# Kernel optimization log

Hardware: AMD Instinct MI355X
Metric: run time of the kernel (lower is better)

Reference implementation:

```python
import jax, jax.numpy as jnp
import numpy as np

N_EMBD = 768
N_HEAD = 12
HEAD_DIM = N_EMBD // N_HEAD


def setup_inputs() -> dict:
    key = jax.random.key(0)
    k1, k2, k3 = jax.random.split(key, 3)
    B, T, C = 4, 2048, N_EMBD
    x = jax.random.normal(k1, (B, T, C), dtype=jnp.float32)
    # c_attn: torch Linear(C, 3C) -> store as (C, 3C) for x @ W
    w_attn = jax.random.normal(k2, (C, 3 * C), dtype=jnp.float32) * (1.0 / np.sqrt(C))
    b_attn = jax.random.normal(k3, (3 * C,), dtype=jnp.float32) * 0.02
    return {"x": x, "w_attn": w_attn, "b_attn": b_attn}


def reference(x, w_attn, b_attn):
    B, T, C = x.shape
    H, D = N_HEAD, HEAD_DIM
    scale = 1.0 / np.sqrt(D).astype(np.float32)

    qkv = x @ w_attn + b_attn                      # (B, T, 3C)
    q, k, v = jnp.split(qkv, 3, axis=-1)
    q = q.reshape(B, T, H, D).transpose(0, 2, 1, 3)  # (B, H, T, D)
    k = k.reshape(B, T, H, D).transpose(0, 2, 1, 3)
    v = v.reshape(B, T, H, D).transpose(0, 2, 1, 3)

    att = jnp.einsum('bhid,bhjd->bhij', q, k) * scale  # (B, H, T, T)
    causal = jnp.tril(jnp.ones((T, T), dtype=bool))
    # masked positions -> -inf -> relu -> 0; kept positions -> relu(scaled score)
    att = jnp.where(causal, jnp.maximum(att, 0.0), 0.0)

    y = jnp.einsum('bhij,bhjd->bhid', att, v)      # (B, H, T, D)
    y = y.transpose(0, 2, 1, 3).reshape(B, T, C)
    return y
```

## Files before the change

### kernel.cpp

```cpp
#include <hip/hip_runtime.h>
#include <hip/hip_bf16.h>

typedef short bf16x8 __attribute__((ext_vector_type(8)));
typedef float f32x4  __attribute__((ext_vector_type(4)));
typedef unsigned short u16x4 __attribute__((ext_vector_type(4)));

#define CDIM   768
#define NQKV   2304
#define MROWS  8192
#define TSEQ   2048
#define HD     64
#define NHEAD  12
#define BHTOT  48

__device__ __forceinline__ unsigned short f2bf(float f) {
    unsigned int x;
    __builtin_memcpy(&x, &f, 4);
    unsigned int r = (x + 0x7fffu + ((x >> 16) & 1u)) >> 16;
    return (unsigned short)r;
}

__device__ __forceinline__ unsigned int pkbf(float a, float b) {
    unsigned int ua, ub;
    __builtin_memcpy(&ua, &a, 4);
    __builtin_memcpy(&ub, &b, 4);
    return __builtin_amdgcn_perm(ua + 0x8000u, ub + 0x8000u, 0x03020706u);
}

__device__ __forceinline__ f32x4 mfma16(bf16x8 a, bf16x8 b, f32x4 c) {
    return __builtin_amdgcn_mfma_f32_16x16x32_bf16(a, b, c, 0, 0, 0);
}

__device__ __forceinline__ void gl_lds16(const unsigned short* g, unsigned short* l) {
    __builtin_amdgcn_global_load_lds(
        (__attribute__((address_space(1))) void*)(g),
        (__attribute__((address_space(3))) void*)(l),
        16, 0, 0);
}

__global__ __launch_bounds__(256) void prep(
    const float* __restrict__ X, const float* __restrict__ W,
    unsigned short* __restrict__ Xb, unsigned short* __restrict__ Wt)
{
    const int tid = threadIdx.x, blk = blockIdx.x;
    if (blk < 432) {
        __shared__ __align__(16) unsigned short tile[64][72];
        const int bx = blk % 36, by = blk / 36;
#pragma unroll
        for (int c = 0; c < 4; c++) {
            int chunk = tid + 256 * c;
            int r = chunk >> 4, cc = chunk & 15;
            f32x4 v = *(const f32x4*)(W + (size_t)(by * 64 + r) * NQKV + bx * 64 + cc * 4);
#pragma unroll
            for (int j = 0; j < 4; j++) tile[cc * 4 + j][r] = f2bf(v[j]);
        }
        __syncthreads();
#pragma unroll
        for (int c = 0; c < 2; c++) {
            int chunk = tid + 256 * c;
            int r = chunk >> 3, cc = chunk & 7;
            bf16x8 v;
#pragma unroll
            for (int j = 0; j < 8; j++) v[j] = (short)tile[r][cc * 8 + j];
            *(bf16x8*)(Wt + (size_t)(bx * 64 + r) * CDIM + by * 64 + cc * 8) = v;
        }
    }
    for (size_t i4 = (size_t)blk * 256 + tid; i4 < (size_t)(MROWS * CDIM / 4);
         i4 += (size_t)448 * 256) {
        f32x4 v = *(const f32x4*)(X + i4 * 4);
        u16x4 o;
#pragma unroll
        for (int j = 0; j < 4; j++) o[j] = f2bf(v[j]);
        *(u16x4*)(Xb + i4 * 4) = o;
    }
}

#define BK 64

__global__ __launch_bounds__(512, 4) void qkv_gemm(
    const unsigned short* __restrict__ X,
    const unsigned short* __restrict__ Wt,
    const float* __restrict__ Bias,
    unsigned short* __restrict__ Q,
    unsigned short* __restrict__ Km,
    unsigned short* __restrict__ Vt)
{
    __shared__ __align__(16) unsigned short As[256 * BK];
    __shared__ __align__(16) unsigned short Bs[128 * BK];
    const int tid  = threadIdx.x;
    const int wave = tid >> 6, lane = tid & 63;
    const int quad = lane >> 4, m16 = lane & 15;
    const int wr = wave >> 1, wc = wave & 1;

    const int t   = blockIdx.x;
    const int xcd = t & 7, s = t >> 3;
    const int m0  = (xcd * 4 + (s & 3)) * 256;
    const int n0  = (s >> 2) * 128;

    f32x4 acc[4][4];
#pragma unroll
    for (int i = 0; i < 4; i++)
#pragma unroll
        for (int j = 0; j < 4; j++) acc[i][j] = f32x4{0.f, 0.f, 0.f, 0.f};

    const unsigned short* xb = X + (size_t)m0 * CDIM;
    const unsigned short* wb = Wt + (size_t)n0 * CDIM;

    const int spos = lane & 7;
    const int rb = m16 & 7;
    int arow[4], brow[2];
#pragma unroll
    for (int c = 0; c < 4; c++) arow[c] = (wave * 256 + c * 64 + lane) >> 3;
#pragma unroll
    for (int c = 0; c < 2; c++) brow[c] = (wave * 128 + c * 64 + lane) >> 3;

    for (int k0 = 0; k0 < CDIM; k0 += BK) {
#pragma unroll
        for (int c = 0; c < 4; c++) {
            int row = arow[c], ch = spos ^ (row & 7);
            gl_lds16(xb + (size_t)row * CDIM + k0 + ch * 8, As + wave * 2048 + c * 512);
        }
#pragma unroll
        for (int c = 0; c < 2; c++) {
            int row = brow[c], ch = spos ^ (row & 7);
            gl_lds16(wb + (size_t)row * CDIM + k0 + ch * 8, Bs + wave * 1024 + c * 512);
        }
        __syncthreads();
#pragma unroll
        for (int ks = 0; ks < 2; ks++) {
            bf16x8 af[4], bfg[4];
#pragma unroll
            for (int u = 0; u < 4; u++) {
                int rowa = wr * 64 + u * 16 + m16;
                int rowb = wc * 64 + u * 16 + m16;
                int pos = (ks * 4 + quad) ^ rb;
                af[u]  = *(const bf16x8*)(As + rowa * 64 + pos * 8);
                bfg[u] = *(const bf16x8*)(Bs + rowb * 64 + pos * 8);
            }
#pragma unroll
            for (int i = 0; i < 4; i++)
#pragma unroll
                for (int j = 0; j < 4; j++)
                    acc[i][j] = mfma16(af[i], bfg[j], acc[i][j]);
        }
        __syncthreads();
    }

    const int region = n0 / CDIM;
    const float qscale = (region == 0) ? 0.125f : 1.0f;
#pragma unroll
    for (int i = 0; i < 4; i++) {
        int row = m0 + wr * 64 + i * 16 + quad * 4;
#pragma unroll
        for (int j = 0; j < 4; j++) {
            int gcol = n0 + wc * 64 + j * 16 + m16;
            int cc = gcol - region * CDIM;
            int h = cc >> 6, d = cc & 63;
            float bv = Bias[gcol];
#pragma unroll
            for (int r = 0; r < 4; r++) {
                int gm = row + r;
                int b = gm >> 11, tq = gm & 2047;
                int bh = b * NHEAD + h;
                unsigned short o = f2bf((acc[i][j][r] + bv) * qscale);
                if (region == 0)      Q[((size_t)bh * TSEQ + tq) * HD + d] = o;
                else if (region == 1) Km[((size_t)bh * TSEQ + tq) * HD + d] = o;
                else                  Vt[((size_t)bh * HD + d) * TSEQ + tq] = o;
            }
        }
    }
}

#define LDSK 0
#define LDSV 8192

__global__ __launch_bounds__(256, 4) void attn(
    const unsigned short* __restrict__ Q,
    const unsigned short* __restrict__ Kmat,
    const unsigned short* __restrict__ Vt,
    float* __restrict__ Out)
{
    __shared__ __align__(16) unsigned short S[16384];

    const int tid  = threadIdx.x;
    const int wave = tid >> 6, lane = tid & 63;
    const int q4 = lane >> 4, m16 = lane & 15;
    const int q8 = m16 >> 2, m3 = m16 & 3;

    const int xcd = blockIdx.x & 7;
    const int idx = blockIdx.x >> 3;
    const int bh  = xcd * 6 + (idx % 6);
    const int it  = 15 - (idx / 6);
    const int i0  = it * 128;

    const unsigned short* qb = Q    + (size_t)bh * TSEQ * HD;
    const unsigned short* kb = Kmat + (size_t)bh * TSEQ * HD;
    const unsigned short* vb = Vt   + (size_t)bh * HD * TSEQ;

    bf16x8 qf[2][2];
#pragma unroll
    for (int si = 0; si < 2; si++)
#pragma unroll
        for (int ks = 0; ks < 2; ks++)
            qf[si][ks] = *(const bf16x8*)(qb +
                (size_t)(i0 + wave * 32 + si * 16 + m16) * HD + ks * 32 + q4 * 8);

    f32x4 oacc[2][4];
#pragma unroll
    for (int si = 0; si < 2; si++)
#pragma unroll
        for (int dn = 0; dn < 4; dn++) oacc[si][dn] = f32x4{0.f, 0.f, 0.f, 0.f};

    const int fr  = ((q8 & 1) << 2) | m3;
    const int kx0 = (q4 ^ fr) * 8;
    const int kx1 = kx0 ^ 32;
    const int krb = (q8 * 8 + m3) * 64;

    for (int jt = 0; jt <= it; jt++) {
        const int j0 = jt * 128;
#pragma unroll
        for (int cc = 0; cc < 4; cc++) {
            int cs = wave * 4 + cc;
            {
                int rowK = cs * 8 + (lane >> 3);
                int chK  = (lane & 7) ^ ((((rowK >> 3) & 1) << 2) | (rowK & 3));
                gl_lds16(kb + (size_t)(j0 + rowK) * HD + chK * 8, &S[LDSK] + cs * 512);
            }
            {
                int dV  = cs * 4 + (lane >> 4);
                int chV = (m16 & 8) | ((m16 ^ dV) & 7);
                gl_lds16(vb + (size_t)dV * TSEQ + j0 + chV * 8, &S[LDSV] + cs * 512);
            }
        }
        __syncthreads();

        const bool diag = (jt == it);
#pragma unroll
        for (int kk = 0; kk < 4; kk++) {
            const int kb0 = kk * 2048 + krb;
            bf16x8 kf_e0 = *(const bf16x8*)(&S[LDSK] + kb0 + kx0);
            bf16x8 kf_e1 = *(const bf16x8*)(&S[LDSK] + kb0 + kx1);
            bf16x8 kf_o0 = *(const bf16x8*)(&S[LDSK] + kb0 + 256 + kx0);
            bf16x8 kf_o1 = *(const bf16x8*)(&S[LDSK] + kb0 + 256 + kx1);

            f32x4 sacc[2][2];
#pragma unroll
            for (int o = 0; o < 2; o++)
#pragma unroll
                for (int si = 0; si < 2; si++) sacc[o][si] = f32x4{0.f, 0.f, 0.f, 0.f};
#pragma unroll
            for (int si = 0; si < 2; si++) {
                sacc[0][si] = mfma16(kf_e0, qf[si][0], sacc[0][si]);
                sacc[0][si] = mfma16(kf_e1, qf[si][1], sacc[0][si]);
                sacc[1][si] = mfma16(kf_o0, qf[si][0], sacc[1][si]);
                sacc[1][si] = mfma16(kf_o1, qf[si][1], sacc[1][si]);
            }

            unsigned int pk[2][2][2];
#pragma unroll
            for (int o = 0; o < 2; o++)
#pragma unroll
                for (int si = 0; si < 2; si++) {
                    f32x4 v = sacc[o][si];
                    if (diag) {
#pragma unroll
                        for (int r = 0; r < 4; r++) {
                            int gj = kk * 32 + q4 * 8 + o * 4 + r;
                            int gi = wave * 32 + si * 16 + m16;
                            if (gj > gi) v[r] = 0.f;
                        }
                    }
#pragma unroll
                    for (int r = 0; r < 4; r++) v[r] = fmaxf(v[r], 0.f);
                    pk[o][si][0] = pkbf(v[0], v[1]);
                    pk[o][si][1] = pkbf(v[2], v[3]);
                }

#pragma unroll
            for (int dn = 0; dn < 4; dn++) {
                int vsw = ((kk * 4 + q4) ^ (m16 & 7)) * 8;
                bf16x8 vf = *(const bf16x8*)(&S[LDSV] + (dn * 16 + m16) * 128 + vsw);
#pragma unroll
                for (int si = 0; si < 2; si++) {
                    union { bf16x8 v; unsigned int u[4]; } af;
                    af.u[0] = pk[0][si][0];
                    af.u[1] = pk[0][si][1];
                    af.u[2] = pk[1][si][0];
                    af.u[3] = pk[1][si][1];
                    oacc[si][dn] = mfma16(af.v, vf, oacc[si][dn]);
                }
            }
        }
        __syncthreads();
    }

    const int b = bh / NHEAD, h = bh % NHEAD;
#pragma unroll
    for (int si = 0; si < 2; si++) {
        int ri = i0 + wave * 32 + si * 16 + q4 * 4;
#pragma unroll
        for (int dn = 0; dn < 4; dn++) {
            int d = dn * 16 + m16;
#pragma unroll
            for (int r = 0; r < 4; r++) {
                Out[((size_t)b * TSEQ + ri + r) * CDIM + h * HD + d] = oacc[si][dn][r];
            }
        }
    }
}

extern "C" void kernel_launch(void* const* d_in, const int* in_sizes, int n_in,
                              void* d_out, int out_size, void* d_ws, size_t ws_size,
                              hipStream_t stream) {
    const float* X    = (const float*)d_in[0];
    const float* W    = (const float*)d_in[1];
    const float* Bias = (const float*)d_in[2];
    float* out = (float*)d_out;

    unsigned short* Xb = (unsigned short*)d_ws;
    unsigned short* Wt = Xb + (size_t)MROWS * CDIM;
    unsigned short* Q  = Wt + (size_t)NQKV * CDIM;
    unsigned short* Km = Q  + (size_t)BHTOT * TSEQ * HD;
    unsigned short* Vt = Km + (size_t)BHTOT * TSEQ * HD;

    hipLaunchKernelGGL(prep, dim3(448), dim3(256), 0, stream, X, W, Xb, Wt);
    hipLaunchKernelGGL(qkv_gemm, dim3(576), dim3(512), 0, stream,
                       Xb, Wt, Bias, Q, Km, Vt);
    hipLaunchKernelGGL(attn, dim3(BHTOT * 16), dim3(256), 0, stream, Q, Km, Vt, out);
}
```

Measured before the change: 178.0 us.

## Double attention query tile to 256 rows with 8 waves sharing K/V tiles

Each attention block now covers 256 query rows with 512 threads (8 waves) instead of 128 rows with 4 waves. Each K/V tile staged in LDS is therefore reused by twice as many query rows, and each wave loads half as many chunks. The causal mask check becomes per-wave, since the diagonal now spans two key tiles. The cost is fewer, larger blocks (384), which gives coarser causal load balancing and wasted MFMA work on fully masked tiles for the lower waves.

Result: no change. 181.3 us (+1.8%).

```diff
diff --git a/kernel.cpp b/kernel.cpp
--- a/kernel.cpp
+++ b/kernel.cpp
@@ -174,7 +174,7 @@
 #define LDSK 0
 #define LDSV 8192
 
-__global__ __launch_bounds__(256, 4) void attn(
+__global__ __launch_bounds__(512, 4) void attn(
     const unsigned short* __restrict__ Q,
     const unsigned short* __restrict__ Kmat,
     const unsigned short* __restrict__ Vt,
@@ -188,10 +188,11 @@
     const int q8 = m16 >> 2, m3 = m16 & 3;
 
     const int xcd = blockIdx.x & 7;
-    const int idx = blockIdx.x >> 3;
-    const int bh  = xcd * 6 + (idx % 6);
-    const int it  = 15 - (idx / 6);
-    const int i0  = it * 128;
+    const int u   = blockIdx.x >> 3;
+    const int bh  = xcd * 6 + (u % 6);
+    const int it2 = 7 - (u / 6);
+    const int i0  = it2 * 256;
+    const int iw  = i0 + wave * 32;
 
     const unsigned short* qb = Q    + (size_t)bh * TSEQ * HD;
     const unsigned short* kb = Kmat + (size_t)bh * TSEQ * HD;
@@ -203,7 +204,7 @@
 #pragma unroll
         for (int ks = 0; ks < 2; ks++)
             qf[si][ks] = *(const bf16x8*)(qb +
-                (size_t)(i0 + wave * 32 + si * 16 + m16) * HD + ks * 32 + q4 * 8);
+                (size_t)(iw + si * 16 + m16) * HD + ks * 32 + q4 * 8);
 
     f32x4 oacc[2][4];
 #pragma unroll
@@ -216,11 +217,12 @@
     const int kx1 = kx0 ^ 32;
     const int krb = (q8 * 8 + m3) * 64;
 
-    for (int jt = 0; jt <= it; jt++) {
+    const int njt = 2 * it2 + 2;
+    for (int jt = 0; jt < njt; jt++) {
         const int j0 = jt * 128;
 #pragma unroll
-        for (int cc = 0; cc < 4; cc++) {
-            int cs = wave * 4 + cc;
+        for (int cc = 0; cc < 2; cc++) {
+            int cs = wave * 2 + cc;
             {
                 int rowK = cs * 8 + (lane >> 3);
                 int chK  = (lane & 7) ^ ((((rowK >> 3) & 1) << 2) | (rowK & 3));
@@ -234,7 +236,7 @@
         }
         __syncthreads();
 
-        const bool diag = (jt == it);
+        const bool needmask = (j0 + 127 > iw);
 #pragma unroll
         for (int kk = 0; kk < 4; kk++) {
             const int kb0 = kk * 2048 + krb;
@@ -262,11 +264,11 @@
 #pragma unroll
                 for (int si = 0; si < 2; si++) {
                     f32x4 v = sacc[o][si];
-                    if (diag) {
+                    if (needmask) {
 #pragma unroll
                         for (int r = 0; r < 4; r++) {
-                            int gj = kk * 32 + q4 * 8 + o * 4 + r;
-                            int gi = wave * 32 + si * 16 + m16;
+                            int gj = j0 + kk * 32 + q4 * 8 + o * 4 + r;
+                            int gi = iw + si * 16 + m16;
                             if (gj > gi) v[r] = 0.f;
                         }
                     }
@@ -282,11 +284,11 @@
                 bf16x8 vf = *(const bf16x8*)(&S[LDSV] + (dn * 16 + m16) * 128 + vsw);
 #pragma unroll
                 for (int si = 0; si < 2; si++) {
-                    union { bf16x8 v; unsigned int u[4]; } af;
-                    af.u[0] = pk[0][si][0];
-                    af.u[1] = pk[0][si][1];
-                    af.u[2] = pk[1][si][0];
-                    af.u[3] = pk[1][si][1];
+                    union { bf16x8 v; unsigned int uu[4]; } af;
+                    af.uu[0] = pk[0][si][0];
+                    af.uu[1] = pk[0][si][1];
+                    af.uu[2] = pk[1][si][0];
+                    af.uu[3] = pk[1][si][1];
                     oacc[si][dn] = mfma16(af.v, vf, oacc[si][dn]);
                 }
             }
@@ -297,7 +299,7 @@
     const int b = bh / NHEAD, h = bh % NHEAD;
 #pragma unroll
     for (int si = 0; si < 2; si++) {
-        int ri = i0 + wave * 32 + si * 16 + q4 * 4;
+        int ri = iw + si * 16 + q4 * 4;
 #pragma unroll
         for (int dn = 0; dn < 4; dn++) {
             int d = dn * 16 + m16;
@@ -326,5 +328,5 @@
     hipLaunchKernelGGL(prep, dim3(448), dim3(256), 0, stream, X, W, Xb, Wt);
     hipLaunchKernelGGL(qkv_gemm, dim3(576), dim3(512), 0, stream,
                        Xb, Wt, Bias, Q, Km, Vt);
-    hipLaunchKernelGGL(attn, dim3(BHTOT * 16), dim3(256), 0, stream, Q, Km, Vt, out);
-}
+    hipLaunchKernelGGL(attn, dim3(384), dim3(512), 0, stream, Q, Km, Vt, out);
+}
```
